# Kernel tuning notes

Measured on AMD Instinct MI355X. Metric: run time of the kernel, lower is better.

The kernel has to match this reference:

```python
import jax, jax.numpy as jnp
import numpy as np

INPUT_SIZE = 32
HIDDEN_SIZE = 64
OUTPUT_SIZE = 8
B, T = 8192, 128


def setup_inputs() -> dict:
    key = jax.random.key(0)
    ks = jax.random.split(key, 7)
    s_ih = 1.0 / np.sqrt(HIDDEN_SIZE)
    return {
        "x": jax.random.normal(ks[0], (B, T, INPUT_SIZE), dtype=jnp.float32),
        "W_ih": jax.random.uniform(ks[1], (4 * HIDDEN_SIZE, INPUT_SIZE), minval=-s_ih, maxval=s_ih),
        "W_hh": jax.random.uniform(ks[2], (4 * HIDDEN_SIZE, HIDDEN_SIZE), minval=-s_ih, maxval=s_ih),
        "b_ih": jax.random.uniform(ks[3], (4 * HIDDEN_SIZE,), minval=-s_ih, maxval=s_ih),
        "b_hh": jax.random.uniform(ks[4], (4 * HIDDEN_SIZE,), minval=-s_ih, maxval=s_ih),
        "W_fc": jax.random.uniform(ks[5], (OUTPUT_SIZE, HIDDEN_SIZE), minval=-s_ih, maxval=s_ih),
        "b_fc": jax.random.uniform(ks[6], (OUTPUT_SIZE,), minval=-s_ih, maxval=s_ih),
    }


def _lstm_last_h(x, W_ih, W_hh, b_ih, b_hh):
    Bc, Tc, _ = x.shape
    H = HIDDEN_SIZE
    # Precompute the input contribution to all gates once: [B, T, 4H]
    x_gates = jnp.einsum("bti,gi->btg", x, W_ih) + b_ih + b_hh

    def step(carry, xg_t):  # xg_t: [B, 4H]
        h, c = carry
        gates = xg_t + h @ W_hh.T
        i = jax.nn.sigmoid(gates[:, 0 * H:1 * H])
        f = jax.nn.sigmoid(gates[:, 1 * H:2 * H])
        g = jnp.tanh(gates[:, 2 * H:3 * H])
        o = jax.nn.sigmoid(gates[:, 3 * H:4 * H])
        c = f * c + i * g
        h = o * jnp.tanh(c)
        return (h, c), None

    h0 = jnp.zeros((Bc, H), dtype=x.dtype)
    c0 = jnp.zeros((Bc, H), dtype=x.dtype)
    (h_T, _), _ = jax.lax.scan(step, (h0, c0), jnp.swapaxes(x_gates, 0, 1))
    return h_T  # [B, H] = out[:, -1, :]


def reference(x, W_ih, W_hh, b_ih, b_hh, W_fc, b_fc):
    h_last = _lstm_last_h(x, W_ih, W_hh, b_ih, b_hh)
    return h_last @ W_fc.T + b_fc  # [B, OUTPUT_SIZE]
```

## Files before the change

### kernel.cpp

```cpp
#include <hip/hip_runtime.h>
#include <stdint.h>


#define T_STEPS 128
#define ISZ 32
#define HSZ 64
#define B_TOT 8192
#define B_TILE 16
#define T_CHUNK 32
#define HPAD 144

typedef short bf16x8 __attribute__((ext_vector_type(8)));
typedef float f32x4 __attribute__((ext_vector_type(4)));

#define LOG2E 1.44269504088896340736f

__device__ __forceinline__ float bf2f(unsigned short s) {
    union { unsigned int u; float f; } v; v.u = ((unsigned int)s) << 16; return v.f;
}
__device__ __forceinline__ unsigned short f2bf(float f) {
    union { float f; unsigned int u; } v; v.f = f;
    unsigned int u = v.u;
    return (unsigned short)((u + 0x7fffu + ((u >> 16) & 1u)) >> 16);
}
__device__ __forceinline__ float sig_pre(float z) {
    return __builtin_amdgcn_rcpf(1.0f + __builtin_amdgcn_exp2f(z));
}

template <bool F32>
__device__ __forceinline__ float ldin(const void* p, size_t i) {
    if (F32) return ((const float*)p)[i];
    return bf2f(((const unsigned short*)p)[i]);
}

template <bool F32>
__device__ __forceinline__ void run_body(
    const void* xv, const void* Wihv, const void* Whhv, const void* bihv,
    const void* bhhv, const void* Wfcv, const void* bfcv, void* outv,
    unsigned short (&hbuf)[2][B_TILE][HPAD],
    unsigned short (&xbuf)[T_CHUNK][B_TILE][40],
    float (&hfin)[B_TILE][HSZ + 4])
{
    const int tid  = threadIdx.x;
    const int wid  = tid >> 6;
    const int lane = tid & 63;
    const int q    = lane >> 4;
    const int tn   = lane & 15;
    const int u    = wid * 16 + tn;
    const int b0   = blockIdx.x * B_TILE;

    bf16x8 wf[4][3];
    f32x4 biasC[4];
    #pragma unroll
    for (int g = 0; g < 4; ++g) {
        const float sc = (g == 2) ? (2.0f * LOG2E) : (-LOG2E);
        const int row = g * HSZ + u;
        #pragma unroll
        for (int j = 0; j < 8; ++j) {
            wf[g][0][j] = (short)f2bf(sc * ldin<F32>(Whhv, row * HSZ + q * 8 + j));
            wf[g][1][j] = (short)f2bf(sc * ldin<F32>(Whhv, row * HSZ + 32 + q * 8 + j));
            wf[g][2][j] = (short)f2bf(sc * ldin<F32>(Wihv, row * ISZ + q * 8 + j));
        }
        const float b = sc * (ldin<F32>(bihv, row) + ldin<F32>(bhhv, row));
        #pragma unroll
        for (int e = 0; e < 4; ++e) biasC[g][e] = b;
    }

    for (int i = tid; i < 2 * B_TILE * HPAD; i += 256) ((unsigned short*)hbuf)[i] = 0;

    float cstS[4] = {0.f, 0.f, 0.f, 0.f};
    float hl[4]   = {0.f, 0.f, 0.f, 0.f};

    for (int tc = 0; tc < T_STEPS / T_CHUNK; ++tc) {
        if (F32) {
            const float* xf = (const float*)xv;
            for (int idx = tid; idx < B_TILE * T_CHUNK * 4; idx += 256) {
                const int m  = idx >> 7;
                const int rm = idx & 127;
                const int tl = rm >> 2;
                const int ch = rm & 3;
                const size_t base = ((size_t)(b0 + m) * T_STEPS + (tc * T_CHUNK + tl)) * ISZ + ch * 8;
                const f32x4 v0 = *(const f32x4*)(xf + base);
                const f32x4 v1 = *(const f32x4*)(xf + base + 4);
                bf16x8 w;
                #pragma unroll
                for (int j = 0; j < 4; ++j) {
                    w[j]     = (short)f2bf(v0[j]);
                    w[4 + j] = (short)f2bf(v1[j]);
                }
                *(bf16x8*)&xbuf[tl][m][ch * 8] = w;
            }
        } else {
            const unsigned short* xu = (const unsigned short*)xv;
            for (int idx = tid; idx < B_TILE * T_CHUNK * 4; idx += 256) {
                const int m  = idx >> 7;
                const int rm = idx & 127;
                const int tl = rm >> 2;
                const int ch = rm & 3;
                const uint4 v = *(const uint4*)(xu + ((size_t)(b0 + m) * T_STEPS + (tc * T_CHUNK + tl)) * ISZ + ch * 8);
                *(uint4*)&xbuf[tl][m][ch * 8] = v;
            }
        }
        __syncthreads();

        bf16x8 axc = *(const bf16x8*)&xbuf[0][tn][q * 8];

        #pragma unroll 4
        for (int tl = 0; tl < T_CHUNK; ++tl) {
            const int t  = tc * T_CHUNK + tl;
            const int rb = t & 1, wb = rb ^ 1;
            const bf16x8 a0  = *(const bf16x8*)&hbuf[rb][tn][q * 8];
            const bf16x8 a1  = *(const bf16x8*)&hbuf[rb][tn][32 + q * 8];
            const bf16x8 axn = *(const bf16x8*)&xbuf[(tl + 1) & (T_CHUNK - 1)][tn][q * 8];

            __builtin_amdgcn_s_setprio(1);
            f32x4 acc[4];
            #pragma unroll
            for (int g = 0; g < 4; ++g)
                acc[g] = __builtin_amdgcn_mfma_f32_16x16x32_bf16(axc, wf[g][2], biasC[g], 0, 0, 0);
            #pragma unroll
            for (int g = 0; g < 4; ++g)
                acc[g] = __builtin_amdgcn_mfma_f32_16x16x32_bf16(a0, wf[g][0], acc[g], 0, 0, 0);
            #pragma unroll
            for (int g = 0; g < 4; ++g)
                acc[g] = __builtin_amdgcn_mfma_f32_16x16x32_bf16(a1, wf[g][1], acc[g], 0, 0, 0);

            #pragma unroll
            for (int r = 0; r < 4; ++r) {
                const float gi  = sig_pre(acc[0][r]);
                const float gf  = sig_pre(acc[1][r]);
                const float rg  = __builtin_amdgcn_rcpf(1.0f + __builtin_amdgcn_exp2f(acc[2][r]));
                const float ggS = __builtin_fmaf(rg, -4.0f * LOG2E, 2.0f * LOG2E);
                const float go  = sig_pre(acc[3][r]);
                cstS[r] = gf * cstS[r] + gi * ggS;
                const float th = 1.0f - 2.0f * __builtin_amdgcn_rcpf(1.0f + __builtin_amdgcn_exp2f(cstS[r]));
                const float hv = go * th;
                hl[r] = hv;
                const int m = q * 4 + r;
                hbuf[wb][m][u] = f2bf(hv);
            }
            __builtin_amdgcn_s_setprio(0);

            axc = axn;
            __syncthreads();
        }
    }

    #pragma unroll
    for (int r = 0; r < 4; ++r) hfin[q * 4 + r][u] = hl[r];
    __syncthreads();
    if (tid < B_TILE * 8) {
        const int m = tid >> 3, j = tid & 7;
        float s = ldin<F32>(bfcv, j);
        #pragma unroll
        for (int k = 0; k < HSZ; ++k) s += hfin[m][k] * ldin<F32>(Wfcv, j * HSZ + k);
        const size_t o = (size_t)(b0 + m) * 8 + j;
        if (F32) ((float*)outv)[o] = s;
        else     ((unsigned short*)outv)[o] = f2bf(s);
    }
}

__global__ __launch_bounds__(256, 2) void lstm_fused(
    const void* __restrict__ x, const void* __restrict__ Wih,
    const void* __restrict__ Whh, const void* __restrict__ bih,
    const void* __restrict__ bhh, const void* __restrict__ Wfc,
    const void* __restrict__ bfc, void* __restrict__ out)
{
    __shared__ unsigned short hbuf[2][B_TILE][HPAD];
    __shared__ unsigned short xbuf[T_CHUNK][B_TILE][40];
    __shared__ float hfin[B_TILE][HSZ + 4];

    const unsigned short* xu = (const unsigned short*)x;
    const int lane = threadIdx.x & 63;
    const unsigned short s0 = xu[lane * 2];
    const unsigned short s1 = xu[lane * 2 + 1];
    const int big = (((s0 >> 7) & 0xFF) >= 0x90) || (((s1 >> 7) & 0xFF) >= 0x90);
    const bool isf32 = __any(big) != 0;

    if (isf32) run_body<true >(x, Wih, Whh, bih, bhh, Wfc, bfc, out, hbuf, xbuf, hfin);
    else       run_body<false>(x, Wih, Whh, bih, bhh, Wfc, bfc, out, hbuf, xbuf, hfin);
}

extern "C" void kernel_launch(void* const* d_in, const int* in_sizes, int n_in,
                              void* d_out, int out_size, void* d_ws, size_t ws_size,
                              hipStream_t stream) {
    lstm_fused<<<dim3(B_TOT / B_TILE), dim3(256), 0, stream>>>(
        d_in[0], d_in[1], d_in[2], d_in[3], d_in[4], d_in[5], d_in[6], d_out);
}
```

Before: 261.0 us.

## Replace chunked LDS staging of x with per-thread register prefetch of next step

Removes the shared-memory xbuf that staged 32 timesteps of x per chunk, along with the chunk-level load and sync phases. Each lane now loads its own x fragment straight from global memory one step ahead into registers and converts it to bf16 in place. This cuts LDS footprint and the per-chunk stalls, but each step now issues a small strided global load whose latency must hide behind a single step of compute.

```diff
diff --git a/kernel.cpp b/kernel.cpp
--- a/kernel.cpp
+++ b/kernel.cpp
@@ -7,7 +7,6 @@
 #define HSZ 64
 #define B_TOT 8192
 #define B_TILE 16
-#define T_CHUNK 32
 #define HPAD 144
 
 typedef short bf16x8 __attribute__((ext_vector_type(8)));
@@ -38,7 +37,6 @@
     const void* xv, const void* Wihv, const void* Whhv, const void* bihv,
     const void* bhhv, const void* Wfcv, const void* bfcv, void* outv,
     unsigned short (&hbuf)[2][B_TILE][HPAD],
-    unsigned short (&xbuf)[T_CHUNK][B_TILE][40],
     float (&hfin)[B_TILE][HSZ + 4])
 {
     const int tid  = threadIdx.x;
@@ -66,84 +64,78 @@
         for (int e = 0; e < 4; ++e) biasC[g][e] = b;
     }
 
+    const size_t xbase = ((size_t)(b0 + tn) * T_STEPS) * ISZ + q * 8;
+
+    bf16x8 pendb;
+    f32x4  pend0, pend1;
+    if (F32) {
+        const float* xf = (const float*)xv + xbase;
+        pend0 = *(const f32x4*)(xf);
+        pend1 = *(const f32x4*)(xf + 4);
+    } else {
+        pendb = *(const bf16x8*)((const unsigned short*)xv + xbase);
+    }
+
     for (int i = tid; i < 2 * B_TILE * HPAD; i += 256) ((unsigned short*)hbuf)[i] = 0;
+    __syncthreads();
 
     float cstS[4] = {0.f, 0.f, 0.f, 0.f};
     float hl[4]   = {0.f, 0.f, 0.f, 0.f};
 
-    for (int tc = 0; tc < T_STEPS / T_CHUNK; ++tc) {
+    #pragma unroll 4
+    for (int t = 0; t < T_STEPS; ++t) {
+        const int rb = t & 1, wb = rb ^ 1;
+        const bf16x8 a0 = *(const bf16x8*)&hbuf[rb][tn][q * 8];
+        const bf16x8 a1 = *(const bf16x8*)&hbuf[rb][tn][32 + q * 8];
+
+        bf16x8 axc;
         if (F32) {
-            const float* xf = (const float*)xv;
-            for (int idx = tid; idx < B_TILE * T_CHUNK * 4; idx += 256) {
-                const int m  = idx >> 7;
-                const int rm = idx & 127;
-                const int tl = rm >> 2;
-                const int ch = rm & 3;
-                const size_t base = ((size_t)(b0 + m) * T_STEPS + (tc * T_CHUNK + tl)) * ISZ + ch * 8;
-                const f32x4 v0 = *(const f32x4*)(xf + base);
-                const f32x4 v1 = *(const f32x4*)(xf + base + 4);
-                bf16x8 w;
-                #pragma unroll
-                for (int j = 0; j < 4; ++j) {
-                    w[j]     = (short)f2bf(v0[j]);
-                    w[4 + j] = (short)f2bf(v1[j]);
-                }
-                *(bf16x8*)&xbuf[tl][m][ch * 8] = w;
+            #pragma unroll
+            for (int j = 0; j < 4; ++j) {
+                axc[j]     = (short)f2bf(pend0[j]);
+                axc[4 + j] = (short)f2bf(pend1[j]);
             }
         } else {
-            const unsigned short* xu = (const unsigned short*)xv;
-            for (int idx = tid; idx < B_TILE * T_CHUNK * 4; idx += 256) {
-                const int m  = idx >> 7;
-                const int rm = idx & 127;
-                const int tl = rm >> 2;
-                const int ch = rm & 3;
-                const uint4 v = *(const uint4*)(xu + ((size_t)(b0 + m) * T_STEPS + (tc * T_CHUNK + tl)) * ISZ + ch * 8);
-                *(uint4*)&xbuf[tl][m][ch * 8] = v;
-            }
+            axc = pendb;
         }
+        const int t1 = (t < T_STEPS - 1) ? t + 1 : t;
+        if (F32) {
+            const float* xf = (const float*)xv + xbase + (size_t)t1 * ISZ;
+            pend0 = *(const f32x4*)(xf);
+            pend1 = *(const f32x4*)(xf + 4);
+        } else {
+            pendb = *(const bf16x8*)((const unsigned short*)xv + xbase + (size_t)t1 * ISZ);
+        }
+
+        __builtin_amdgcn_s_setprio(1);
+        f32x4 acc[4];
+        #pragma unroll
+        for (int g = 0; g < 4; ++g)
+            acc[g] = __builtin_amdgcn_mfma_f32_16x16x32_bf16(axc, wf[g][2], biasC[g], 0, 0, 0);
+        #pragma unroll
+        for (int g = 0; g < 4; ++g)
+            acc[g] = __builtin_amdgcn_mfma_f32_16x16x32_bf16(a0, wf[g][0], acc[g], 0, 0, 0);
+        #pragma unroll
+        for (int g = 0; g < 4; ++g)
+            acc[g] = __builtin_amdgcn_mfma_f32_16x16x32_bf16(a1, wf[g][1], acc[g], 0, 0, 0);
+
+        #pragma unroll
+        for (int r = 0; r < 4; ++r) {
+            const float gi  = sig_pre(acc[0][r]);
+            const float gf  = sig_pre(acc[1][r]);
+            const float rg  = __builtin_amdgcn_rcpf(1.0f + __builtin_amdgcn_exp2f(acc[2][r]));
+            const float ggS = __builtin_fmaf(rg, -4.0f * LOG2E, 2.0f * LOG2E);
+            const float go  = sig_pre(acc[3][r]);
+            cstS[r] = gf * cstS[r] + gi * ggS;
+            const float th = 1.0f - 2.0f * __builtin_amdgcn_rcpf(1.0f + __builtin_amdgcn_exp2f(cstS[r]));
+            const float hv = go * th;
+            hl[r] = hv;
+            const int m = q * 4 + r;
+            hbuf[wb][m][u] = f2bf(hv);
+        }
+        __builtin_amdgcn_s_setprio(0);
+
         __syncthreads();
-
-        bf16x8 axc = *(const bf16x8*)&xbuf[0][tn][q * 8];
-
-        #pragma unroll 4
-        for (int tl = 0; tl < T_CHUNK; ++tl) {
-            const int t  = tc * T_CHUNK + tl;
-            const int rb = t & 1, wb = rb ^ 1;
-            const bf16x8 a0  = *(const bf16x8*)&hbuf[rb][tn][q * 8];
-            const bf16x8 a1  = *(const bf16x8*)&hbuf[rb][tn][32 + q * 8];
-            const bf16x8 axn = *(const bf16x8*)&xbuf[(tl + 1) & (T_CHUNK - 1)][tn][q * 8];
-
-            __builtin_amdgcn_s_setprio(1);
-            f32x4 acc[4];
-            #pragma unroll
-            for (int g = 0; g < 4; ++g)
-                acc[g] = __builtin_amdgcn_mfma_f32_16x16x32_bf16(axc, wf[g][2], biasC[g], 0, 0, 0);
-            #pragma unroll
-            for (int g = 0; g < 4; ++g)
-                acc[g] = __builtin_amdgcn_mfma_f32_16x16x32_bf16(a0, wf[g][0], acc[g], 0, 0, 0);
-            #pragma unroll
-            for (int g = 0; g < 4; ++g)
-                acc[g] = __builtin_amdgcn_mfma_f32_16x16x32_bf16(a1, wf[g][1], acc[g], 0, 0, 0);
-
-            #pragma unroll
-            for (int r = 0; r < 4; ++r) {
-                const float gi  = sig_pre(acc[0][r]);
-                const float gf  = sig_pre(acc[1][r]);
-                const float rg  = __builtin_amdgcn_rcpf(1.0f + __builtin_amdgcn_exp2f(acc[2][r]));
-                const float ggS = __builtin_fmaf(rg, -4.0f * LOG2E, 2.0f * LOG2E);
-                const float go  = sig_pre(acc[3][r]);
-                cstS[r] = gf * cstS[r] + gi * ggS;
-                const float th = 1.0f - 2.0f * __builtin_amdgcn_rcpf(1.0f + __builtin_amdgcn_exp2f(cstS[r]));
-                const float hv = go * th;
-                hl[r] = hv;
-                const int m = q * 4 + r;
-                hbuf[wb][m][u] = f2bf(hv);
-            }
-            __builtin_amdgcn_s_setprio(0);
-
-            axc = axn;
-            __syncthreads();
-        }
     }
 
     #pragma unroll
@@ -167,7 +159,6 @@
     const void* __restrict__ bfc, void* __restrict__ out)
 {
     __shared__ unsigned short hbuf[2][B_TILE][HPAD];
-    __shared__ unsigned short xbuf[T_CHUNK][B_TILE][40];
     __shared__ float hfin[B_TILE][HSZ + 4];
 
     const unsigned short* xu = (const unsigned short*)x;
@@ -177,8 +168,8 @@
     const int big = (((s0 >> 7) & 0xFF) >= 0x90) || (((s1 >> 7) & 0xFF) >= 0x90);
     const bool isf32 = __any(big) != 0;
 
-    if (isf32) run_body<true >(x, Wih, Whh, bih, bhh, Wfc, bfc, out, hbuf, xbuf, hfin);
-    else       run_body<false>(x, Wih, Whh, bih, bhh, Wfc, bfc, out, hbuf, xbuf, hfin);
+    if (isf32) run_body<true >(x, Wih, Whh, bih, bhh, Wfc, bfc, out, hbuf, hfin);
+    else       run_body<false>(x, Wih, Whh, bih, bhh, Wfc, bfc, out, hbuf, hfin);
 }
 
 extern "C" void kernel_launch(void* const* d_in, const int* in_sizes, int n_in,
```

After: 259.9 us. No clear change (-0.4%).
